# Optimization experiments

Hardware: AMD Instinct MI355X
Metric: run time of the kernel (lower is better)

The kernel has to match this reference:

```python
import jax, jax.numpy as jnp
import numpy as np
from jax import lax

C = 768
SHIFT_DISTANCES = (1, 2, 3)


def _layernorm(x, g, b, eps=1e-5):
    m = jnp.mean(x, axis=-1, keepdims=True)
    v = jnp.mean((x - m) ** 2, axis=-1, keepdims=True)
    return (x - m) * lax.rsqrt(v + eps) * g + b


def setup_inputs() -> dict:
    key = jax.random.key(0)
    ks = jax.random.split(key, 16)
    B, T, N = 8, 16, 197
    inp = {
        "x": jax.random.normal(ks[0], (B * T, N, C), dtype=jnp.float32),
        "ln_g": jnp.ones((C,), jnp.float32),
        "ln_b": jnp.zeros((C,), jnp.float32),
        "gate_w": jax.random.normal(ks[1], (C, C), jnp.float32) * 0.02,
        "gate_b": jnp.zeros((C,), jnp.float32),
        "proj_w1": jax.random.normal(ks[2], (C, C), jnp.float32) * 0.02,
        "proj_b1": jnp.zeros((C,), jnp.float32),
        "proj_w2": jax.random.normal(ks[3], (C, C), jnp.float32) * 0.02,
        "proj_b2": jnp.zeros((C,), jnp.float32),
        "fusion_w": jnp.ones((len(SHIFT_DISTANCES),), jnp.float32),
        "num_frames": T,
    }
    for i, d in enumerate(SHIFT_DISTANCES):
        k = 2 * d + 1
        # depthwise Conv1d weight: (out=C, in/groups=1, k)
        inp[f"conv_w{i}"] = jax.random.normal(ks[4 + i], (C, 1, k), jnp.float32) * (1.0 / np.sqrt(k))
        inp[f"conv_b{i}"] = jnp.zeros((C,), jnp.float32)
    return inp


def _branch(x4, conv_w, conv_b, d, ln_g, ln_b, gate_w, gate_b):
    # x4: [B, T, N, C]
    B, T, N, Cc = x4.shape
    p = Cc // 3  # past / future split; static gets the remainder
    x_norm = jax.nn.relu(_layernorm(x4, ln_g, ln_b))
    # [B, T, N, C] -> [B*N, C, T] for depthwise conv over time
    x_1d = x_norm.transpose(0, 2, 3, 1).reshape(B * N, Cc, T)
    feat = lax.conv_general_dilated(
        x_1d, conv_w, window_strides=(1,), padding=[(d, d)],
        dimension_numbers=("NCH", "OIH", "NCH"), feature_group_count=Cc,
    ) + conv_b[None, :, None]
    feat = feat.reshape(B, N, Cc, T).transpose(0, 3, 1, 2)  # [B, T, N, C]
    gate = jax.nn.sigmoid(jnp.einsum("btnc,cd->btnd", feat, gate_w) + gate_b)
    y = gate * x4  # channelwise split-and-multiply fuses into one op
    y_past, y_future, y_static = y[..., :p], y[..., p:2 * p], y[..., 2 * p:]
    s = min(d, T)
    out_past = jnp.pad(y_past[:, s:], ((0, 0), (0, s), (0, 0), (0, 0)))  # lshift
    out_future = jnp.pad(y_future[:, :T - s], ((0, 0), (s, 0), (0, 0), (0, 0)))  # rshift
    return jnp.concatenate([out_past, out_future, y_static], axis=-1)


def reference(x, ln_g, ln_b, gate_w, gate_b, proj_w1, proj_b1, proj_w2, proj_b2,
              fusion_w, conv_w0, conv_b0, conv_w1, conv_b1, conv_w2, conv_b2,
              num_frames):
    B_T, N, Cc = x.shape
    T = num_frames
    B = B_T // T
    x4 = x.reshape(B, T, N, Cc)
    convs = [(conv_w0, conv_b0), (conv_w1, conv_b1), (conv_w2, conv_b2)]
    outs = jnp.stack([
        _branch(x4, cw, cb, d, ln_g, ln_b, gate_w, gate_b)
        for (cw, cb), d in zip(convs, SHIFT_DISTANCES)
    ], axis=0)  # [3, B, T, N, C]
    w = jax.nn.softmax(fusion_w)[:, None, None, None, None]
    fused = jnp.sum(w * outs, axis=0).reshape(B_T, N, Cc)
    h = jnp.einsum("bnc,cd->bnd", fused, proj_w1) + proj_b1
    h = jax.nn.gelu(h, approximate=False)
    h = jnp.einsum("bnc,cd->bnd", h, proj_w2) + proj_b2
    return x + h
```

## Files before the change

### kernel.cpp

```cpp
#include <hip/hip_runtime.h>
#include <math.h>


#define MROWS 25216
#define CD    768
#define NTOK  197
#define TFR   16

typedef __attribute__((ext_vector_type(8))) short short8;
typedef __attribute__((ext_vector_type(4))) float floatx4;
typedef unsigned int u32;

__device__ __forceinline__ unsigned short f2bf(float f) {
    union { float f; unsigned u; } v; v.f = f;
    unsigned r = v.u + 0x7FFFu + ((v.u >> 16) & 1u);
    return (unsigned short)(r >> 16);
}
__device__ __forceinline__ float bf2f(unsigned short h) {
    union { unsigned u; float f; } v; v.u = ((unsigned)h) << 16;
    return v.f;
}

__device__ __forceinline__ void gl2lds16(const void* g, void* l) {
    __builtin_amdgcn_global_load_lds(
        (__attribute__((address_space(1))) void*)(unsigned long long)g,
        (__attribute__((address_space(3))) void*)(u32)(unsigned long long)l,
        16, 0, 0);
}

__global__ __launch_bounds__(256)
void ln_relu_kernel(const float* __restrict__ x, const float* __restrict__ g,
                    const float* __restrict__ b, unsigned short* __restrict__ xn,
                    unsigned short* __restrict__ xb) {
    int row = blockIdx.x;
    int tid = threadIdx.x;
    const float* xr = x + (size_t)row * CD;
    float v0 = xr[tid], v1 = xr[tid + 256], v2 = xr[tid + 512];
    float s = v0 + v1 + v2;
    __shared__ float red[8];
#pragma unroll
    for (int off = 32; off; off >>= 1) s += __shfl_down(s, off, 64);
    int lane = tid & 63, w = tid >> 6;
    if (lane == 0) red[w] = s;
    __syncthreads();
    float mean = (red[0] + red[1] + red[2] + red[3]) * (1.0f / CD);
    float d0 = v0 - mean, d1 = v1 - mean, d2 = v2 - mean;
    float s2 = d0 * d0 + d1 * d1 + d2 * d2;
#pragma unroll
    for (int off = 32; off; off >>= 1) s2 += __shfl_down(s2, off, 64);
    if (lane == 0) red[4 + w] = s2;
    __syncthreads();
    float var = (red[4] + red[5] + red[6] + red[7]) * (1.0f / CD);
    float inv = rsqrtf(var + 1e-5f);
    unsigned short* xo = xn + (size_t)row * CD;
    unsigned short* xc = xb + (size_t)row * CD;
    float o0 = fmaxf(d0 * inv * g[tid]       + b[tid],       0.0f);
    float o1 = fmaxf(d1 * inv * g[tid + 256] + b[tid + 256], 0.0f);
    float o2 = fmaxf(d2 * inv * g[tid + 512] + b[tid + 512], 0.0f);
    xo[tid] = f2bf(o0); xo[tid + 256] = f2bf(o1); xo[tid + 512] = f2bf(o2);
    xc[tid] = f2bf(v0); xc[tid + 256] = f2bf(v1); xc[tid + 512] = f2bf(v2);
}

template <int D>
__device__ __forceinline__
void dw_body(const unsigned short* __restrict__ xn, const float* __restrict__ cw,
             const float* __restrict__ cb, unsigned short* __restrict__ feat) {
    constexpr int KK = 2 * D + 1;
    int gid = blockIdx.x * 256 + threadIdx.x;
    int bn = gid / 96;
    int cg = gid - bn * 96;
    int c0 = cg * 8;
    int b = bn / NTOK;
    size_t base = ((size_t)b * TFR * NTOK + (bn - b * NTOK)) * CD + c0;
    const size_t tstride = (size_t)NTOK * CD;

    short8 u[TFR];
#pragma unroll
    for (int t = 0; t < TFR; ++t)
        u[t] = *(const short8*)(xn + base + (size_t)t * tstride);

    float wgt[8][KK], bb[8];
#pragma unroll
    for (int q = 0; q < 8; ++q) {
        bb[q] = cb[c0 + q];
#pragma unroll
        for (int j = 0; j < KK; ++j) wgt[q][j] = cw[(c0 + q) * KK + j];
    }

#pragma unroll
    for (int t = 0; t < TFR; ++t) {
        float acc[8];
#pragma unroll
        for (int q = 0; q < 8; ++q) acc[q] = bb[q];
#pragma unroll
        for (int j = 0; j < KK; ++j) {
            int tj = t + j - D;
            if (tj < 0 || tj >= TFR) continue;
#pragma unroll
            for (int q = 0; q < 8; ++q)
                acc[q] += bf2f((unsigned short)u[tj][q]) * wgt[q][j];
        }
        short8 o;
#pragma unroll
        for (int q = 0; q < 8; ++q) o[q] = (short)f2bf(acc[q]);
        *(short8*)(feat + base + (size_t)t * tstride) = o;
    }
}

__global__ __launch_bounds__(256)
void dwconv_all(const unsigned short* __restrict__ xn,
                const float* __restrict__ cw0, const float* __restrict__ cb0,
                const float* __restrict__ cw1, const float* __restrict__ cb1,
                const float* __restrict__ cw2, const float* __restrict__ cb2,
                unsigned short* __restrict__ f1, unsigned short* __restrict__ f2,
                unsigned short* __restrict__ f3) {
    if (blockIdx.y == 0)      dw_body<1>(xn, cw0, cb0, f1);
    else if (blockIdx.y == 1) dw_body<2>(xn, cw1, cb1, f2);
    else                      dw_body<3>(xn, cw2, cb2, f3);
}

__global__ __launch_bounds__(256)
void wprep3_kernel(const float* __restrict__ w0, const float* __restrict__ w1,
                   const float* __restrict__ w2, unsigned short* __restrict__ t0,
                   unsigned short* __restrict__ t1, unsigned short* __restrict__ t2) {
    const float* w = blockIdx.y == 0 ? w0 : blockIdx.y == 1 ? w1 : w2;
    unsigned short* wt = blockIdx.y == 0 ? t0 : blockIdx.y == 1 ? t1 : t2;
    int gid = blockIdx.x * 256 + threadIdx.x;
    int n = gid / CD, k = gid - n * CD;
    wt[gid] = f2bf(w[(size_t)k * CD + n]);
}

__global__ __launch_bounds__(256)
void fuse_kernel(const unsigned short* __restrict__ y1,
                 const unsigned short* __restrict__ y2,
                 const unsigned short* __restrict__ y3,
                 unsigned short* __restrict__ fused) {
    int gid = blockIdx.x * 256 + threadIdx.x;
    int m = gid / 96;
    int kk = (gid - m * 96) * 8;
    int t = (m / NTOK) & 15;
    float vals[8] = {0.f, 0.f, 0.f, 0.f, 0.f, 0.f, 0.f, 0.f};
    const unsigned short* ys[3] = {y1, y2, y3};
#pragma unroll
    for (int d = 1; d <= 3; ++d) {
        int src; bool ok;
        if (kk < 256)      { src = m + d * NTOK; ok = (t + d) < TFR; }
        else if (kk < 512) { src = m - d * NTOK; ok = (t - d) >= 0; }
        else               { src = m;            ok = true; }
        if (ok) {
            short8 u = *(const short8*)(ys[d - 1] + (size_t)src * CD + kk);
#pragma unroll
            for (int e = 0; e < 8; ++e) vals[e] += bf2f((unsigned short)u[e]);
        }
    }
    short8 o;
#pragma unroll
    for (int e = 0; e < 8; ++e) o[e] = (short)f2bf(vals[e]);
    *(short8*)(fused + (size_t)m * CD + kk) = o;
}

template <int EPI>
__global__ __launch_bounds__(256)
void gemm_kernel(const unsigned short* __restrict__ A,
                 const unsigned short* __restrict__ Bt,
                 const float* __restrict__ bias,
                 const unsigned short* __restrict__ xb,
                 const float* __restrict__ xf,
                 float* __restrict__ outf,
                 unsigned short* __restrict__ outh,
                 const float* __restrict__ fw,
                 int widx) {
    __shared__ __align__(16) char smem[65536];
    unsigned short (*As)[128 * 32] = (unsigned short (*)[128 * 32])smem;
    unsigned short (*Bs)[128 * 32] = (unsigned short (*)[128 * 32])(smem + 32768);
    float (*fE)[132] = (float (*)[132])smem;

    int tid  = threadIdx.x;
    int m0   = blockIdx.x * 128;
    int n0   = blockIdx.y * 128;
    int wave = tid >> 6, lane = tid & 63;
    int wm   = (wave >> 1) * 64, wn = (wave & 1) * 64;
    int quad = lane >> 4, l16 = lane & 15;
    int r4   = lane >> 2;
    int ckx  = (((lane & 3) ^ ((lane >> 3) & 3)) * 8);
    int rdsl = (quad ^ ((l16 >> 1) & 3)) * 8;

    const size_t arow = (size_t)(m0 + wave * 16 + r4) * CD + ckx;
    const size_t brow = (size_t)(n0 + wave * 16 + r4) * CD + ckx;
    const size_t skip = (size_t)64 * CD;

    floatx4 acc[4][4];
#pragma unroll
    for (int i = 0; i < 4; ++i)
#pragma unroll
        for (int j = 0; j < 4; ++j) acc[i][j] = (floatx4){0.f, 0.f, 0.f, 0.f};

    auto stage = [&](int t, int b) {
        const size_t ko = (size_t)t * 32;
#pragma unroll
        for (int h = 0; h < 2; ++h) {
            gl2lds16(A  + arow + h * skip + ko, &As[b][(wave + h * 4) * 512]);
            gl2lds16(Bt + brow + h * skip + ko, &Bs[b][(wave + h * 4) * 512]);
        }
    };
    auto compute = [&](int b) {
        short8 af[4], bfr[4];
#pragma unroll
        for (int i = 0; i < 4; ++i) af[i]  = *(const short8*)(&As[b][(wm + i * 16 + l16) * 32 + rdsl]);
#pragma unroll
        for (int j = 0; j < 4; ++j) bfr[j] = *(const short8*)(&Bs[b][(wn + j * 16 + l16) * 32 + rdsl]);
#pragma unroll
        for (int i = 0; i < 4; ++i)
#pragma unroll
            for (int j = 0; j < 4; ++j)
                acc[i][j] = __builtin_amdgcn_mfma_f32_16x16x32_bf16(af[i], bfr[j], acc[i][j], 0, 0, 0);
    };

    constexpr int NT = CD / 32;
    stage(0, 0);
    stage(1, 1);
    stage(2, 2);
    for (int t = 0; t < NT - 2; ++t) {
        asm volatile("s_waitcnt vmcnt(8)" ::: "memory");
        __builtin_amdgcn_s_barrier();
        __builtin_amdgcn_sched_barrier(0);
        if (t + 3 < NT) stage(t + 3, (t + 3) & 3);
        compute(t & 3);
    }
    asm volatile("s_waitcnt vmcnt(4)" ::: "memory");
    __builtin_amdgcn_s_barrier();
    __builtin_amdgcn_sched_barrier(0);
    compute((NT - 2) & 3);
    asm volatile("s_waitcnt vmcnt(0)" ::: "memory");
    __builtin_amdgcn_s_barrier();
    __builtin_amdgcn_sched_barrier(0);
    compute((NT - 1) & 3);

    float wd = 0.f;
    if (EPI == 0) {
        float f0 = fw[0], f1 = fw[1], f2 = fw[2];
        float mx = fmaxf(f0, fmaxf(f1, f2));
        float e0 = expf(f0 - mx), e1 = expf(f1 - mx), e2 = expf(f2 - mx);
        float inv = 1.f / (e0 + e1 + e2);
        wd = (widx == 0 ? e0 : widx == 1 ? e1 : e2) * inv;
    }

#pragma unroll
    for (int p = 0; p < 2; ++p) {
        __syncthreads();
        if (wm == p * 64) {
#pragma unroll
            for (int j = 0; j < 4; ++j) {
                int col = wn + j * 16 + l16;
                float bc = bias[n0 + col];
#pragma unroll
                for (int i = 0; i < 4; ++i)
#pragma unroll
                    for (int r = 0; r < 4; ++r)
                        fE[i * 16 + quad * 4 + r][col] = acc[i][j][r] + bc;
            }
        }
        __syncthreads();
#pragma unroll
        for (int it = 0; it < 4; ++it) {
            int lr   = it * 16 + (tid >> 4);
            int cg   = tid & 15;
            size_t grow = (size_t)(m0 + p * 64 + lr);
            int gcol = n0 + cg * 8;
            size_t idx = grow * CD + gcol;
            floatx4 v0 = *(const floatx4*)&fE[lr][cg * 8];
            floatx4 v1 = *(const floatx4*)&fE[lr][cg * 8 + 4];
            if (EPI == 0) {
                short8 xv = *(const short8*)(xb + idx);
                short8 o;
#pragma unroll
                for (int e = 0; e < 8; ++e) {
                    float vv = e < 4 ? v0[e] : v1[e - 4];
                    float gte = 1.f / (1.f + expf(-vv));
                    o[e] = (short)f2bf(wd * gte * bf2f((unsigned short)xv[e]));
                }
                *(short8*)(outh + idx) = o;
            } else if (EPI == 1) {
                short8 o;
#pragma unroll
                for (int e = 0; e < 8; ++e) {
                    float vv = e < 4 ? v0[e] : v1[e - 4];
                    float gl = 0.5f * vv * (1.0f + erff(vv * 0.70710678118f));
                    o[e] = (short)f2bf(gl);
                }
                *(short8*)(outh + idx) = o;
            } else {
                floatx4 x0 = *(const floatx4*)(xf + idx);
                floatx4 x1 = *(const floatx4*)(xf + idx + 4);
#pragma unroll
                for (int e = 0; e < 4; ++e) { v0[e] += x0[e]; v1[e] += x1[e]; }
                *(floatx4*)(outf + idx)     = v0;
                *(floatx4*)(outf + idx + 4) = v1;
            }
        }
    }
}

extern "C" void kernel_launch(void* const* d_in, const int* in_sizes, int n_in,
                              void* d_out, int out_size, void* d_ws, size_t ws_size,
                              hipStream_t stream) {
    const float* x      = (const float*)d_in[0];
    const float* ln_g   = (const float*)d_in[1];
    const float* ln_b   = (const float*)d_in[2];
    const float* gate_w = (const float*)d_in[3];
    const float* gate_b = (const float*)d_in[4];
    const float* pw1    = (const float*)d_in[5];
    const float* pb1    = (const float*)d_in[6];
    const float* pw2    = (const float*)d_in[7];
    const float* pb2    = (const float*)d_in[8];
    const float* fw     = (const float*)d_in[9];
    const float* cw[3]  = {(const float*)d_in[11], (const float*)d_in[13], (const float*)d_in[15]};
    const float* cb[3]  = {(const float*)d_in[12], (const float*)d_in[14], (const float*)d_in[16]};

    char* ws = (char*)d_ws;
    const size_t SB = (size_t)MROWS * CD * 2;
    unsigned short* gwt  = (unsigned short*)(ws + 0);
    unsigned short* p1t  = (unsigned short*)(ws + 1179648);
    unsigned short* p2t  = (unsigned short*)(ws + 2359296);
    unsigned short* xn   = (unsigned short*)(ws + 3538944);
    unsigned short* xb   = (unsigned short*)(ws + 3538944 + SB);
    unsigned short* f1   = (unsigned short*)(ws + 3538944 + 2 * SB);
    unsigned short* f2   = (unsigned short*)(ws + 3538944 + 3 * SB);
    unsigned short* f3   = (unsigned short*)(ws + 3538944 + 4 * SB);
    unsigned short* y1    = xn;
    unsigned short* y2    = f1;
    unsigned short* y3    = f2;
    unsigned short* fused = f3;
    unsigned short* h1    = xn;

    dim3 wg(2304, 3);
    wprep3_kernel<<<wg, 256, 0, stream>>>(gate_w, pw1, pw2, gwt, p1t, p2t);
    ln_relu_kernel<<<MROWS, 256, 0, stream>>>(x, ln_g, ln_b, xn, xb);

    dim3 dg(591, 3);
    dwconv_all<<<dg, 256, 0, stream>>>(xn, cw[0], cb[0], cw[1], cb[1], cw[2], cb[2],
                                       f1, f2, f3);

    dim3 gg(197, 6);
    gemm_kernel<0><<<gg, 256, 0, stream>>>(f1, gwt, gate_b, xb, nullptr,
                                           nullptr, y1, fw, 0);
    gemm_kernel<0><<<gg, 256, 0, stream>>>(f2, gwt, gate_b, xb, nullptr,
                                           nullptr, y2, fw, 1);
    gemm_kernel<0><<<gg, 256, 0, stream>>>(f3, gwt, gate_b, xb, nullptr,
                                           nullptr, y3, fw, 2);

    fuse_kernel<<<9456, 256, 0, stream>>>(y1, y2, y3, fused);

    gemm_kernel<1><<<gg, 256, 0, stream>>>(fused, p1t, pb1, nullptr, nullptr,
                                           nullptr, h1, nullptr, 0);
    gemm_kernel<2><<<gg, 256, 0, stream>>>(h1, p2t, pb2, nullptr, x,
                                           (float*)d_out, nullptr, nullptr, 0);
}
```

Baseline: 554.9 us.

## Merge three gate GEMMs into one launch and interleave loads with MFMA half-steps

The three per-branch gate GEMMs become a single launch over a 3x taller grid, treating the contiguous conv outputs as one A matrix and routing each block's output to a per-branch buffer. This reduces launch overhead and wave-quantization tail. The k-loop is also split into two halves, each issuing half the next-stage loads before a prioritized MFMA burst, with an added barrier between halves. The change needs two extra workspace buffers and adds a barrier per k-step.

```diff
diff --git a/kernel.cpp b/kernel.cpp
--- a/kernel.cpp
+++ b/kernel.cpp
@@ -167,9 +167,10 @@
                  const unsigned short* __restrict__ xb,
                  const float* __restrict__ xf,
                  float* __restrict__ outf,
-                 unsigned short* __restrict__ outh,
-                 const float* __restrict__ fw,
-                 int widx) {
+                 unsigned short* __restrict__ outh0,
+                 unsigned short* __restrict__ outh1,
+                 unsigned short* __restrict__ outh2,
+                 const float* __restrict__ fw) {
     __shared__ __align__(16) char smem[65536];
     unsigned short (*As)[128 * 32] = (unsigned short (*)[128 * 32])smem;
     unsigned short (*Bs)[128 * 32] = (unsigned short (*)[128 * 32])(smem + 32768);
@@ -178,6 +179,7 @@
     int tid  = threadIdx.x;
     int m0   = blockIdx.x * 128;
     int n0   = blockIdx.y * 128;
+    int widx = blockIdx.x / (MROWS / 128);
     int wave = tid >> 6, lane = tid & 63;
     int wm   = (wave >> 1) * 64, wn = (wave & 1) * 64;
     int quad = lane >> 4, l16 = lane & 15;
@@ -195,28 +197,49 @@
 #pragma unroll
         for (int j = 0; j < 4; ++j) acc[i][j] = (floatx4){0.f, 0.f, 0.f, 0.f};
 
-    auto stage = [&](int t, int b) {
+    auto stage_h = [&](int t, int b, int h) {
         const size_t ko = (size_t)t * 32;
-#pragma unroll
-        for (int h = 0; h < 2; ++h) {
-            gl2lds16(A  + arow + h * skip + ko, &As[b][(wave + h * 4) * 512]);
-            gl2lds16(Bt + brow + h * skip + ko, &Bs[b][(wave + h * 4) * 512]);
-        }
+        gl2lds16(A  + arow + h * skip + ko, &As[b][(wave + h * 4) * 512]);
+        gl2lds16(Bt + brow + h * skip + ko, &Bs[b][(wave + h * 4) * 512]);
     };
-    auto compute = [&](int b) {
+    auto stage = [&](int t, int b) { stage_h(t, b, 0); stage_h(t, b, 1); };
+
+    constexpr int NT = CD / 32;
+
+    auto kstep = [&](int t, bool doStage) {
+        int b = t & 3;
         short8 af[4], bfr[4];
 #pragma unroll
-        for (int i = 0; i < 4; ++i) af[i]  = *(const short8*)(&As[b][(wm + i * 16 + l16) * 32 + rdsl]);
-#pragma unroll
-        for (int j = 0; j < 4; ++j) bfr[j] = *(const short8*)(&Bs[b][(wn + j * 16 + l16) * 32 + rdsl]);
-#pragma unroll
         for (int i = 0; i < 4; ++i)
-#pragma unroll
-            for (int j = 0; j < 4; ++j)
-                acc[i][j] = __builtin_amdgcn_mfma_f32_16x16x32_bf16(af[i], bfr[j], acc[i][j], 0, 0, 0);
+            af[i] = *(const short8*)(&As[b][(wm + i * 16 + l16) * 32 + rdsl]);
+        bfr[0] = *(const short8*)(&Bs[b][(wn + 0 * 16 + l16) * 32 + rdsl]);
+        bfr[1] = *(const short8*)(&Bs[b][(wn + 1 * 16 + l16) * 32 + rdsl]);
+        if (doStage) stage_h(t + 3, (t + 3) & 3, 0);
+        asm volatile("s_waitcnt lgkmcnt(0)" ::: "memory");
+        __builtin_amdgcn_sched_barrier(0);
+        __builtin_amdgcn_s_setprio(1);
+#pragma unroll
+        for (int i = 0; i < 4; ++i) {
+            acc[i][0] = __builtin_amdgcn_mfma_f32_16x16x32_bf16(af[i], bfr[0], acc[i][0], 0, 0, 0);
+            acc[i][1] = __builtin_amdgcn_mfma_f32_16x16x32_bf16(af[i], bfr[1], acc[i][1], 0, 0, 0);
+        }
+        __builtin_amdgcn_s_setprio(0);
+        __builtin_amdgcn_s_barrier();
+        __builtin_amdgcn_sched_barrier(0);
+        bfr[2] = *(const short8*)(&Bs[b][(wn + 2 * 16 + l16) * 32 + rdsl]);
+        bfr[3] = *(const short8*)(&Bs[b][(wn + 3 * 16 + l16) * 32 + rdsl]);
+        if (doStage) stage_h(t + 3, (t + 3) & 3, 1);
+        asm volatile("s_waitcnt lgkmcnt(0)" ::: "memory");
+        __builtin_amdgcn_sched_barrier(0);
+        __builtin_amdgcn_s_setprio(1);
+#pragma unroll
+        for (int i = 0; i < 4; ++i) {
+            acc[i][2] = __builtin_amdgcn_mfma_f32_16x16x32_bf16(af[i], bfr[2], acc[i][2], 0, 0, 0);
+            acc[i][3] = __builtin_amdgcn_mfma_f32_16x16x32_bf16(af[i], bfr[3], acc[i][3], 0, 0, 0);
+        }
+        __builtin_amdgcn_s_setprio(0);
     };
 
-    constexpr int NT = CD / 32;
     stage(0, 0);
     stage(1, 1);
     stage(2, 2);
@@ -224,26 +247,28 @@
         asm volatile("s_waitcnt vmcnt(8)" ::: "memory");
         __builtin_amdgcn_s_barrier();
         __builtin_amdgcn_sched_barrier(0);
-        if (t + 3 < NT) stage(t + 3, (t + 3) & 3);
-        compute(t & 3);
+        kstep(t, t + 3 < NT);
     }
     asm volatile("s_waitcnt vmcnt(4)" ::: "memory");
     __builtin_amdgcn_s_barrier();
     __builtin_amdgcn_sched_barrier(0);
-    compute((NT - 2) & 3);
+    kstep(NT - 2, false);
     asm volatile("s_waitcnt vmcnt(0)" ::: "memory");
     __builtin_amdgcn_s_barrier();
     __builtin_amdgcn_sched_barrier(0);
-    compute((NT - 1) & 3);
+    kstep(NT - 1, false);
 
     float wd = 0.f;
+    unsigned short* outh = outh0;
     if (EPI == 0) {
         float f0 = fw[0], f1 = fw[1], f2 = fw[2];
         float mx = fmaxf(f0, fmaxf(f1, f2));
         float e0 = expf(f0 - mx), e1 = expf(f1 - mx), e2 = expf(f2 - mx);
         float inv = 1.f / (e0 + e1 + e2);
         wd = (widx == 0 ? e0 : widx == 1 ? e1 : e2) * inv;
-    }
+        outh = widx == 0 ? outh0 : widx == 1 ? outh1 : outh2;
+    }
+    const size_t lshift = (size_t)widx * MROWS * CD;
 
 #pragma unroll
     for (int p = 0; p < 2; ++p) {
@@ -267,7 +292,7 @@
             int cg   = tid & 15;
             size_t grow = (size_t)(m0 + p * 64 + lr);
             int gcol = n0 + cg * 8;
-            size_t idx = grow * CD + gcol;
+            size_t idx = grow * CD + gcol - lshift;
             floatx4 v0 = *(const floatx4*)&fE[lr][cg * 8];
             floatx4 v1 = *(const floatx4*)&fE[lr][cg * 8 + 4];
             if (EPI == 0) {
@@ -341,18 +366,17 @@
     dwconv_all<<<dg, 256, 0, stream>>>(xn, cw[0], cb[0], cw[1], cb[1], cw[2], cb[2],
                                        f1, f2, f3);
 
+    dim3 gg3(591, 6);
+    unsigned short* y2s = (unsigned short*)(ws + 3538944 + 5 * SB);
+    unsigned short* y3s = (unsigned short*)(ws + 3538944 + 6 * SB);
+    gemm_kernel<0><<<gg3, 256, 0, stream>>>(f1, gwt, gate_b, xb, nullptr,
+                                            nullptr, y1, y2s, y3s, fw);
+
+    fuse_kernel<<<9456, 256, 0, stream>>>(y1, y2s, y3s, fused);
+
     dim3 gg(197, 6);
-    gemm_kernel<0><<<gg, 256, 0, stream>>>(f1, gwt, gate_b, xb, nullptr,
-                                           nullptr, y1, fw, 0);
-    gemm_kernel<0><<<gg, 256, 0, stream>>>(f2, gwt, gate_b, xb, nullptr,
-                                           nullptr, y2, fw, 1);
-    gemm_kernel<0><<<gg, 256, 0, stream>>>(f3, gwt, gate_b, xb, nullptr,
-                                           nullptr, y3, fw, 2);
-
-    fuse_kernel<<<9456, 256, 0, stream>>>(y1, y2, y3, fused);
-
     gemm_kernel<1><<<gg, 256, 0, stream>>>(fused, p1t, pb1, nullptr, nullptr,
-                                           nullptr, h1, nullptr, 0);
+                                           nullptr, h1, nullptr, nullptr, nullptr);
     gemm_kernel<2><<<gg, 256, 0, stream>>>(h1, p2t, pb2, nullptr, x,
-                                           (float*)d_out, nullptr, nullptr, 0);
-}
+                                           (float*)d_out, nullptr, nullptr, nullptr, nullptr);
+}
```

Result: no change. 549.5 us (-1.0%).
